# Kernel optimization log

Measured on AMD Instinct MI355X. Metric: run time of the kernel, lower is better.

Reference implementation:

```python
import jax, jax.numpy as jnp
import numpy as np

N, E = 100000, 1600000
IN, HID, NCLS = 128, 128, 64


def setup_inputs() -> dict:
    key = jax.random.key(0)
    ks = jax.random.split(key, 8)
    x = jax.random.normal(ks[0], (N, IN), jnp.float32)
    edge_index = jax.random.randint(ks[1], (2, E), 0, N, dtype=jnp.int32)
    s1 = 1.0 / np.sqrt(IN)
    s2 = 1.0 / np.sqrt(HID)
    return {
        "x": x,
        "edge_index": edge_index,
        "Wl1": jax.random.uniform(ks[2], (IN, HID), jnp.float32, -s1, s1),
        "Wr1": jax.random.uniform(ks[3], (IN, HID), jnp.float32, -s1, s1),
        "b1": jnp.zeros((HID,), jnp.float32),
        "Wl2": jax.random.uniform(ks[4], (HID, NCLS), jnp.float32, -s2, s2),
        "Wr2": jax.random.uniform(ks[5], (HID, NCLS), jnp.float32, -s2, s2),
        "b2": jnp.zeros((NCLS,), jnp.float32),
    }


def _sage_conv(x, src, dst, inv_deg, Wl, Wr, b):
    # mean-aggregate neighbor features at each destination node (PyG SAGEConv)
    agg = jax.ops.segment_sum(x[src], dst, num_segments=N)  # [N, d]
    agg = agg * inv_deg[:, None]
    # out = lin_l(mean_j x_j) + lin_r(x_i); bias lives in lin_l
    return agg @ Wl + x @ Wr + b


def reference(x, edge_index, Wl1, Wr1, b1, Wl2, Wr2, b2):
    src, dst = edge_index[0], edge_index[1]
    deg = jax.ops.segment_sum(jnp.ones((E,), jnp.float32), dst, num_segments=N)
    inv_deg = 1.0 / jnp.maximum(deg, 1.0)
    h = _sage_conv(x, src, dst, inv_deg, Wl1, Wr1, b1)
    h = jax.nn.relu(h)
    # dropout is identity at inference (training=False)
    h = _sage_conv(h, src, dst, inv_deg, Wl2, Wr2, b2)
    return jax.nn.log_softmax(h, axis=1)
```

## Files before the change

kernel.cpp:

```cpp
#include <hip/hip_runtime.h>
#include <hip/hip_bf16.h>


typedef __attribute__((ext_vector_type(8))) short short8;
typedef __attribute__((ext_vector_type(4))) float f32x4;
typedef __attribute__((ext_vector_type(2))) float f32x2;

#define NPB 512
#define BCAP 16384
#define CHUNK 8192

__device__ __forceinline__ ushort f2bf(float f) {
    unsigned u = __float_as_uint(f);
    return (ushort)((u + 0x7fff + ((u >> 16) & 1)) >> 16);
}
__device__ __forceinline__ float bflo(unsigned v) { return __uint_as_float(v << 16); }
__device__ __forceinline__ float bfhi(unsigned v) { return __uint_as_float(v & 0xffff0000u); }
__device__ __forceinline__ unsigned pk4bf(float a, float b) {
    unsigned r;
    asm("v_cvt_pk_bf16_f32 %0, %1, %2" : "=v"(r) : "v"(a), "v"(b));
    return r;
}
__device__ __forceinline__ f32x2 pkadd(f32x2 a, f32x2 b) {
    f32x2 r;
    asm("v_pk_add_f32 %0, %1, %2" : "=v"(r) : "v"(a), "v"(b));
    return r;
}
__device__ __forceinline__ f32x2 shflx2(f32x2 v, int m) {
    f32x2 r; r[0] = __shfl_xor(v[0], m); r[1] = __shfl_xor(v[1], m); return r;
}

__device__ __forceinline__ void wfrag_one(const float* W, ushort* Wf, int i, int COLS) {
    int j = i & 7, m = (i >> 3) & 15, kc = (i >> 7) & 15, ct = i >> 11;
    Wf[i] = f2bf(W[(kc * 8 + j) * COLS + ct * 16 + m]);
}

__global__ void __launch_bounds__(256)
k1_scatter_cvtw(const int* __restrict__ src, const int* __restrict__ dst,
                int* __restrict__ bcount, unsigned* __restrict__ bbuf, int E, int NSC,
                const float* __restrict__ Wl1, const float* __restrict__ Wr1,
                const float* __restrict__ Wl2, const float* __restrict__ Wr2,
                ushort* __restrict__ Wf_l1, ushort* __restrict__ Wf_r1,
                ushort* __restrict__ Wf_l2, ushort* __restrict__ Wf_r2) {
    int tid = threadIdx.x;
    if ((int)blockIdx.x >= NSC) {
        int i = ((int)blockIdx.x - NSC) * 256 + tid;
        if (i < 16384)       wfrag_one(Wl1, Wf_l1, i, 128);
        else if (i < 32768)  wfrag_one(Wr1, Wf_r1, i - 16384, 128);
        else if (i < 40960)  wfrag_one(Wl2, Wf_l2, i - 32768, 64);
        else if (i < 49152)  wfrag_one(Wr2, Wf_r2, i - 40960, 64);
        return;
    }
    __shared__ unsigned entry[CHUNK];
    __shared__ unsigned char ebkt[CHUNK];
    __shared__ int lhist[256], lbase[256], lcur[256];
    lhist[tid] = 0;
    __syncthreads();
    int e0 = blockIdx.x * CHUNK;
    int cnt = min(CHUNK, E - e0);
    int nv = cnt >> 2;
    for (int t = tid; t < nv; t += 256) {
        int4 d4 = ((const int4*)(dst + e0))[t];
        int4 s4 = ((const int4*)(src + e0))[t];
        int i = t * 4;
        int b0 = d4.x >> 9, b1 = d4.y >> 9, b2 = d4.z >> 9, b3 = d4.w >> 9;
        entry[i + 0] = ((unsigned)s4.x << 9) | (unsigned)(d4.x & 511);
        entry[i + 1] = ((unsigned)s4.y << 9) | (unsigned)(d4.y & 511);
        entry[i + 2] = ((unsigned)s4.z << 9) | (unsigned)(d4.z & 511);
        entry[i + 3] = ((unsigned)s4.w << 9) | (unsigned)(d4.w & 511);
        ebkt[i + 0] = (unsigned char)b0; ebkt[i + 1] = (unsigned char)b1;
        ebkt[i + 2] = (unsigned char)b2; ebkt[i + 3] = (unsigned char)b3;
        atomicAdd(&lhist[b0], 1); atomicAdd(&lhist[b1], 1);
        atomicAdd(&lhist[b2], 1); atomicAdd(&lhist[b3], 1);
    }
    for (int i = (nv << 2) + tid; i < cnt; i += 256) {
        int d = dst[e0 + i], s = src[e0 + i];
        int b = d >> 9;
        entry[i] = ((unsigned)s << 9) | (unsigned)(d & 511);
        ebkt[i] = (unsigned char)b;
        atomicAdd(&lhist[b], 1);
    }
    __syncthreads();
    int h = lhist[tid];
    lbase[tid] = (h > 0) ? atomicAdd(&bcount[tid], h) : 0;
    lcur[tid] = 0;
    __syncthreads();
    for (int i = tid; i < cnt; i += 256) {
        int b = ebkt[i];
        int o = atomicAdd(&lcur[b], 1);
        bbuf[(long)b * BCAP + lbase[b] + o] = entry[i];
    }
}

template <int CTOT>
__device__ __forceinline__ void stage_weights(const ushort* __restrict__ Wfl,
                                              const ushort* __restrict__ Wfr,
                                              ushort* dst, int tid) {
    constexpr int HALF = CTOT / 2;
    constexpr int ITERS = (CTOT * 2) / 8192;
#pragma unroll
    for (int r = 0; r < ITERS; ++r) {
        int u = r * 4096 + tid * 8;
        const ushort* s = (u < HALF) ? (Wfl + u) : (Wfr + (u - HALF));
        *(short8*)(dst + u) = *(const short8*)s;
    }
}

template <int COLS, bool F32IN>
__device__ __forceinline__ void proj_tile(int bid, int tid,
                            const void* __restrict__ xin,
                            const ushort* Wl, const ushort* Wr,
                            const float* __restrict__ bias,
                            unsigned char* __restrict__ p8, ushort* __restrict__ q, int N) {
    constexpr int CT = COLS / 16;
    int wave = tid >> 6, lane = tid & 63;
    int quad = lane >> 4, m = lane & 15;
    long row0 = (long)bid * 128 + wave * 16;
    long node = row0 + m;
    long arow = (node < N) ? node : (N - 1);

    f32x4 accp[CT], accq[CT];
#pragma unroll
    for (int ct = 0; ct < CT; ++ct) { accp[ct] = (f32x4)0.0f; accq[ct] = (f32x4)0.0f; }

#pragma unroll
    for (int kk = 0; kk < 128; kk += 32) {
        short8 b;
        if (F32IN) {
            const float* xf = (const float*)xin + arow * 128 + kk + quad * 8;
            float4 f0 = *(const float4*)xf;
            float4 f1 = *(const float4*)(xf + 4);
            union { short8 s; unsigned u[4]; } bu;
            bu.u[0] = pk4bf(f0.x, f0.y);
            bu.u[1] = pk4bf(f0.z, f0.w);
            bu.u[2] = pk4bf(f1.x, f1.y);
            bu.u[3] = pk4bf(f1.z, f1.w);
            b = bu.s;
        } else {
            b = *(const short8*)((const ushort*)xin + arow * 128 + kk + quad * 8);
        }
        int kc = (kk >> 3) + quad;
#pragma unroll
        for (int ct = 0; ct < CT; ++ct) {
            int boff = ((ct * 16 + kc) * 16 + m) * 8;
            short8 al = *(const short8*)(Wl + boff);
            short8 ar = *(const short8*)(Wr + boff);
            accp[ct] = __builtin_amdgcn_mfma_f32_16x16x32_bf16(al, b, accp[ct], 0, 0, 0);
            accq[ct] = __builtin_amdgcn_mfma_f32_16x16x32_bf16(ar, b, accq[ct], 0, 0, 0);
        }
    }

    if (node <= N) {
        unsigned msk = (node == N) ? 0u : ~0u;
#pragma unroll
        for (int ct = 0; ct < CT; ++ct) {
            int c0 = ct * 16 + quad * 4;
            float4 bv = *(const float4*)(bias + c0);
            float q0 = accq[ct][0] + bv.x, q1 = accq[ct][1] + bv.y;
            float q2 = accq[ct][2] + bv.z, q3 = accq[ct][3] + bv.w;
            unsigned w = (unsigned)__builtin_amdgcn_cvt_pk_fp8_f32(accp[ct][0], accp[ct][1], 0, false);
            w = (unsigned)__builtin_amdgcn_cvt_pk_fp8_f32(accp[ct][2], accp[ct][3], (int)w, true);
            *(unsigned*)(p8 + node * COLS + c0) = w & msk;
            uint2 qw; qw.x = pk4bf(q0, q1) & msk; qw.y = pk4bf(q2, q3) & msk;
            *(uint2*)(q + node * COLS + c0) = qw;
        }
    }
}

__global__ void __launch_bounds__(512, 4)
k2_csr_proj1(const unsigned* __restrict__ bbuf, const int* __restrict__ bcount,
             int* __restrict__ rsd,
             float* __restrict__ inv_deg, int* __restrict__ ssrc,
             int NBcsr, int PGRID, int NT, int N,
             const float* __restrict__ x,
             const ushort* __restrict__ Wfl, const ushort* __restrict__ Wfr,
             const float* __restrict__ bias,
             unsigned char* __restrict__ p8, ushort* __restrict__ q) {
    extern __shared__ char smem[];
    int tid = threadIdx.x;
    if ((int)blockIdx.x >= NBcsr) {
        ushort* wsm = (ushort*)smem;
        stage_weights<2 * 128 * 128>(Wfl, Wfr, wsm, tid);
        __syncthreads();
        for (int t = (int)blockIdx.x - NBcsr; t < NT; t += PGRID)
            proj_tile<128, true>(t, tid, x, wsm, wsm + 128 * 128, bias, p8, q, N);
        return;
    }
    int* sdeg = (int*)smem;
    int* lcur = sdeg + NPB;
    int* wsum = lcur + NPB;
    unsigned* ecache = (unsigned*)(wsum + 16);
    const int ECAPV = 3836;
    int b = blockIdx.x;
    int node0 = b * NPB;
    sdeg[tid] = 0;
    __syncthreads();
    int cnt = bcount[b];
    long base = (long)b * BCAP;
    const unsigned* bb = bbuf + base;
    int nv = cnt >> 2;
    int cnv = min(nv, ECAPV);
    for (int t = tid; t < nv; t += 512) {
        uint4 e = ((const uint4*)bb)[t];
        if (t < cnv) ((uint4*)ecache)[t] = e;
        atomicAdd(&sdeg[e.x & 511], 1);
        atomicAdd(&sdeg[e.y & 511], 1);
        atomicAdd(&sdeg[e.z & 511], 1);
        atomicAdd(&sdeg[e.w & 511], 1);
    }
    for (int i = (nv << 2) + tid; i < cnt; i += 512)
        atomicAdd(&sdeg[bb[i] & 511], 1);
    __syncthreads();
    int lane = tid & 63, wv = tid >> 6;
    int c0 = sdeg[tid];
    int dp = (c0 + 15) & ~15;
    int v = dp;
#pragma unroll
    for (int o = 1; o < 64; o <<= 1) {
        int t = __shfl_up(v, o);
        if (lane >= o) v += t;
    }
    if (lane == 63) wsum[wv] = v;
    __syncthreads();
    int add = 0;
    for (int w = 0; w < wv; ++w) add += wsum[w];
    int rs0 = v + add - dp;
    lcur[tid] = rs0;
    if (node0 + tid < N) {
        int2 rv; rv.x = (int)(base + rs0); rv.y = dp;
        *(int2*)(rsd + 2 * (node0 + tid)) = rv;
        inv_deg[node0 + tid] = 1.0f / (float)(c0 > 1 ? c0 : 1);
    }
    __syncthreads();
    for (int t = tid; t < cnv; t += 512) {
        uint4 e = ((const uint4*)ecache)[t];
        int p0 = atomicAdd(&lcur[e.x & 511], 1);
        int p1 = atomicAdd(&lcur[e.y & 511], 1);
        int p2 = atomicAdd(&lcur[e.z & 511], 1);
        int p3 = atomicAdd(&lcur[e.w & 511], 1);
        ssrc[base + p0] = (int)(e.x >> 9);
        ssrc[base + p1] = (int)(e.y >> 9);
        ssrc[base + p2] = (int)(e.z >> 9);
        ssrc[base + p3] = (int)(e.w >> 9);
    }
    for (int t = cnv + tid; t < nv; t += 512) {
        uint4 e = ((const uint4*)bb)[t];
        int p0 = atomicAdd(&lcur[e.x & 511], 1);
        int p1 = atomicAdd(&lcur[e.y & 511], 1);
        int p2 = atomicAdd(&lcur[e.z & 511], 1);
        int p3 = atomicAdd(&lcur[e.w & 511], 1);
        ssrc[base + p0] = (int)(e.x >> 9);
        ssrc[base + p1] = (int)(e.y >> 9);
        ssrc[base + p2] = (int)(e.z >> 9);
        ssrc[base + p3] = (int)(e.w >> 9);
    }
    for (int i = (nv << 2) + tid; i < cnt; i += 512) {
        unsigned w = bb[i];
        int pos = atomicAdd(&lcur[w & 511], 1);
        ssrc[base + pos] = (int)(w >> 9);
    }
    for (int i = c0; i < dp; ++i) ssrc[base + rs0 + i] = N;
    if (tid == 511) {
        int tot = v + add;
        for (int k = 0; k < 16; ++k) ssrc[base + tot + k] = N;
    }
}

__global__ void __launch_bounds__(256)
agg_relu_kernel(const unsigned char* __restrict__ p8,
                const ushort* __restrict__ q,
                const int* __restrict__ ssrc,
                const int* __restrict__ rsd,
                const float* __restrict__ inv_deg,
                ushort* __restrict__ hb, int N) {
    int wave = threadIdx.x >> 6, lane = threadIdx.x & 63;
    int n = blockIdx.x * 4 + wave;
    if (n >= N) return;
    int g = lane >> 4, lm = lane & 15;
    int2 rv = *(const int2*)(rsd + 2 * n);
    int start = rv.x, dp = rv.y;
    float iv = inv_deg[n];
    uint4 qv = make_uint4(0u, 0u, 0u, 0u);
    if (g == 0) qv = *(const uint4*)(q + (long)n * 128 + lm * 8);
    const int* sp = ssrc + start;
    const unsigned char* pb = p8 + lm * 8;
    f32x2 a0 = (f32x2)0.f, a1 = (f32x2)0.f, a2 = (f32x2)0.f, a3 = (f32x2)0.f;
    int4 s = *(const int4*)(sp + 4 * g);
    for (int j = 0; j < dp; j += 16) {
        uint2 v0 = *(const uint2*)(pb + (unsigned)s.x * 128u);
        uint2 v1 = *(const uint2*)(pb + (unsigned)s.y * 128u);
        uint2 v2 = *(const uint2*)(pb + (unsigned)s.z * 128u);
        uint2 v3 = *(const uint2*)(pb + (unsigned)s.w * 128u);
        s = *(const int4*)(sp + j + 16 + 4 * g);
        a0 = pkadd(a0, __builtin_amdgcn_cvt_pk_f32_fp8((int)v0.x, false));
        a1 = pkadd(a1, __builtin_amdgcn_cvt_pk_f32_fp8((int)v0.x, true));
        a2 = pkadd(a2, __builtin_amdgcn_cvt_pk_f32_fp8((int)v0.y, false));
        a3 = pkadd(a3, __builtin_amdgcn_cvt_pk_f32_fp8((int)v0.y, true));
        a0 = pkadd(a0, __builtin_amdgcn_cvt_pk_f32_fp8((int)v1.x, false));
        a1 = pkadd(a1, __builtin_amdgcn_cvt_pk_f32_fp8((int)v1.x, true));
        a2 = pkadd(a2, __builtin_amdgcn_cvt_pk_f32_fp8((int)v1.y, false));
        a3 = pkadd(a3, __builtin_amdgcn_cvt_pk_f32_fp8((int)v1.y, true));
        a0 = pkadd(a0, __builtin_amdgcn_cvt_pk_f32_fp8((int)v2.x, false));
        a1 = pkadd(a1, __builtin_amdgcn_cvt_pk_f32_fp8((int)v2.x, true));
        a2 = pkadd(a2, __builtin_amdgcn_cvt_pk_f32_fp8((int)v2.y, false));
        a3 = pkadd(a3, __builtin_amdgcn_cvt_pk_f32_fp8((int)v2.y, true));
        a0 = pkadd(a0, __builtin_amdgcn_cvt_pk_f32_fp8((int)v3.x, false));
        a1 = pkadd(a1, __builtin_amdgcn_cvt_pk_f32_fp8((int)v3.x, true));
        a2 = pkadd(a2, __builtin_amdgcn_cvt_pk_f32_fp8((int)v3.y, false));
        a3 = pkadd(a3, __builtin_amdgcn_cvt_pk_f32_fp8((int)v3.y, true));
    }
    a0 = pkadd(a0, shflx2(a0, 16)); a1 = pkadd(a1, shflx2(a1, 16));
    a2 = pkadd(a2, shflx2(a2, 16)); a3 = pkadd(a3, shflx2(a3, 16));
    a0 = pkadd(a0, shflx2(a0, 32)); a1 = pkadd(a1, shflx2(a1, 32));
    a2 = pkadd(a2, shflx2(a2, 32)); a3 = pkadd(a3, shflx2(a3, 32));
    if (g == 0) {
        float h0 = fmaxf(a0[0] * iv + bflo(qv.x), 0.f);
        float h1 = fmaxf(a0[1] * iv + bfhi(qv.x), 0.f);
        float h2 = fmaxf(a1[0] * iv + bflo(qv.y), 0.f);
        float h3 = fmaxf(a1[1] * iv + bfhi(qv.y), 0.f);
        float h4 = fmaxf(a2[0] * iv + bflo(qv.z), 0.f);
        float h5 = fmaxf(a2[1] * iv + bfhi(qv.z), 0.f);
        float h6 = fmaxf(a3[0] * iv + bflo(qv.w), 0.f);
        float h7 = fmaxf(a3[1] * iv + bfhi(qv.w), 0.f);
        uint4 hw;
        hw.x = pk4bf(h0, h1); hw.y = pk4bf(h2, h3);
        hw.z = pk4bf(h4, h5); hw.w = pk4bf(h6, h7);
        *(uint4*)(hb + (long)n * 128 + lm * 8) = hw;
    }
}

__global__ void __launch_bounds__(512, 4)
proj2_kernel(const ushort* __restrict__ hb,
             const ushort* __restrict__ Wfl, const ushort* __restrict__ Wfr,
             const float* __restrict__ bias,
             unsigned char* __restrict__ u8, ushort* __restrict__ v, int N) {
    __shared__ ushort wsm[2 * 64 * 128];
    stage_weights<2 * 64 * 128>(Wfl, Wfr, wsm, (int)threadIdx.x);
    __syncthreads();
    proj_tile<64, false>((int)blockIdx.x, (int)threadIdx.x, hb, wsm, wsm + 64 * 128,
                         bias, u8, v, N);
}

__global__ void __launch_bounds__(256)
agg_lsm_kernel(const unsigned char* __restrict__ u8,
               const ushort* __restrict__ v,
               const int* __restrict__ ssrc,
               const int* __restrict__ rsd,
               const float* __restrict__ inv_deg,
               float* __restrict__ out, int N) {
    int wave = threadIdx.x >> 6, lane = threadIdx.x & 63;
    int n = blockIdx.x * 4 + wave;
    if (n >= N) return;
    int g = lane >> 4, lm = lane & 15;
    int2 rv = *(const int2*)(rsd + 2 * n);
    int start = rv.x, dp = rv.y;
    float iv = inv_deg[n];
    uint2 vv2 = *(const uint2*)(v + (long)n * 64 + lm * 4);
    const int* sp = ssrc + start;
    const unsigned char* ub = u8 + lm * 4;
    f32x2 a0 = (f32x2)0.f, a1 = (f32x2)0.f;
    int4 s = *(const int4*)(sp + 4 * g);
    for (int j = 0; j < dp; j += 16) {
        unsigned v0 = *(const unsigned*)(ub + (unsigned)s.x * 64u);
        unsigned v1 = *(const unsigned*)(ub + (unsigned)s.y * 64u);
        unsigned v2 = *(const unsigned*)(ub + (unsigned)s.z * 64u);
        unsigned v3 = *(const unsigned*)(ub + (unsigned)s.w * 64u);
        s = *(const int4*)(sp + j + 16 + 4 * g);
        a0 = pkadd(a0, __builtin_amdgcn_cvt_pk_f32_fp8((int)v0, false));
        a1 = pkadd(a1, __builtin_amdgcn_cvt_pk_f32_fp8((int)v0, true));
        a0 = pkadd(a0, __builtin_amdgcn_cvt_pk_f32_fp8((int)v1, false));
        a1 = pkadd(a1, __builtin_amdgcn_cvt_pk_f32_fp8((int)v1, true));
        a0 = pkadd(a0, __builtin_amdgcn_cvt_pk_f32_fp8((int)v2, false));
        a1 = pkadd(a1, __builtin_amdgcn_cvt_pk_f32_fp8((int)v2, true));
        a0 = pkadd(a0, __builtin_amdgcn_cvt_pk_f32_fp8((int)v3, false));
        a1 = pkadd(a1, __builtin_amdgcn_cvt_pk_f32_fp8((int)v3, true));
    }
    a0 = pkadd(a0, shflx2(a0, 16)); a1 = pkadd(a1, shflx2(a1, 16));
    a0 = pkadd(a0, shflx2(a0, 32)); a1 = pkadd(a1, shflx2(a1, 32));

    float z0 = a0[0] * iv + bflo(vv2.x), z1 = a0[1] * iv + bfhi(vv2.x);
    float z2 = a1[0] * iv + bflo(vv2.y), z3 = a1[1] * iv + bfhi(vv2.y);
    float mx = fmaxf(fmaxf(z0, z1), fmaxf(z2, z3));
#pragma unroll
    for (int o = 8; o > 0; o >>= 1) mx = fmaxf(mx, __shfl_xor(mx, o));
    float e = (__expf(z0 - mx) + __expf(z1 - mx)) + (__expf(z2 - mx) + __expf(z3 - mx));
#pragma unroll
    for (int o = 8; o > 0; o >>= 1) e += __shfl_xor(e, o);
    float ls = mx + __logf(e);
    if (g == 0) {
        float4 o0;
        o0.x = z0 - ls; o0.y = z1 - ls; o0.z = z2 - ls; o0.w = z3 - ls;
        *(float4*)(out + (long)n * 64 + lm * 4) = o0;
    }
}

extern "C" void kernel_launch(void* const* d_in, const int* in_sizes, int n_in,
                              void* d_out, int out_size, void* d_ws, size_t ws_size,
                              hipStream_t stream) {
    const float* x   = (const float*)d_in[0];
    const int*   ei  = (const int*)d_in[1];
    const float* Wl1 = (const float*)d_in[2];
    const float* Wr1 = (const float*)d_in[3];
    const float* b1  = (const float*)d_in[4];
    const float* Wl2 = (const float*)d_in[5];
    const float* Wr2 = (const float*)d_in[6];
    const float* b2  = (const float*)d_in[7];

    const int N = in_sizes[0] / 128;
    const int E = in_sizes[1] / 2;
    const int* src = ei;
    const int* dst = ei + E;
    const int NB = (N + NPB - 1) / NPB;
    const int NSC = (E + CHUNK - 1) / CHUNK;

    size_t off = 0;
    auto take = [&](size_t nbytes) -> void* {
        void* ptr = (void*)((char*)d_ws + off);
        off += (nbytes + 255) & ~(size_t)255;
        return ptr;
    };
    int*      bcount    = (int*)take((size_t)NB * 4);
    unsigned* bbuf      = (unsigned*)take((size_t)NB * BCAP * 4);
    int*      rsd       = (int*)take((size_t)N * 8);
    float*    inv_deg   = (float*)take((size_t)N * 4);
    int*      ssrc      = (int*)take((size_t)NB * BCAP * 4);
    unsigned char* p8   = (unsigned char*)take((size_t)(N + 1) * 128);
    ushort*   q         = (ushort*)take((size_t)(N + 1) * 128 * 2);
    ushort*   hb        = (ushort*)take((size_t)N * 128 * 2);
    ushort*   Wf_l1     = (ushort*)take(128 * 128 * 2);
    ushort*   Wf_r1     = (ushort*)take(128 * 128 * 2);
    ushort*   Wf_l2     = (ushort*)take(64 * 128 * 2);
    ushort*   Wf_r2     = (ushort*)take(64 * 128 * 2);
    unsigned char* u8 = p8;
    ushort*        v  = q;
    (void)ws_size; (void)n_in; (void)out_size;

    static bool attr_set = false;
    if (!attr_set) {
        hipFuncSetAttribute((const void*)k2_csr_proj1,
                            hipFuncAttributeMaxDynamicSharedMemorySize, 65536);
        attr_set = true;
    }

    hipMemsetAsync(bcount, 0, (size_t)NB * 4, stream);

    k1_scatter_cvtw<<<NSC + 192, 256, 0, stream>>>(src, dst, bcount, bbuf, E, NSC,
                                                   Wl1, Wr1, Wl2, Wr2,
                                                   Wf_l1, Wf_r1, Wf_l2, Wf_r2);

    const int PGRID = 316;
    const int NT = (N + 127) / 128;
    k2_csr_proj1<<<NB + PGRID, 512, 65536, stream>>>(bbuf, bcount, rsd, inv_deg, ssrc,
                                                     NB, PGRID, NT, N, x,
                                                     Wf_l1, Wf_r1, b1, p8, q);

    agg_relu_kernel<<<(N + 3) / 4, 256, 0, stream>>>(p8, q, ssrc, rsd, inv_deg, hb, N);

    proj2_kernel<<<(N + 127) / 128, 512, 0, stream>>>(hb, Wf_l2, Wf_r2, b2, u8, v, N);
    agg_lsm_kernel<<<(N + 3) / 4, 256, 0, stream>>>(u8, v, ssrc, rsd, inv_deg,
                                                    (float*)d_out, N);
}
```

Baseline: 246.9 us.

## Pre-convert x to bf16 in scatter kernel and use one projection tile per block

The fp32-to-bf16 conversion of x moves out of the layer-1 projection and into extra blocks of the first scatter kernel, which write a bf16 copy of x. The projection blocks in the CSR kernel then read bf16 directly, and the persistent grid of 316 blocks looping over tiles becomes one block per 128-row tile. This shortens the projection tiles that overlap with CSR construction. In exchange, 256 blocks must stream the full 51 MB x tensor and write a 25 MB bf16 copy inside the scatter kernel, which adds total traffic and workspace.

Result: no change. 247.1 us (+0.1%).

```diff
diff --git a/kernel.cpp b/kernel.cpp
--- a/kernel.cpp
+++ b/kernel.cpp
@@ -41,7 +41,8 @@
                 const float* __restrict__ Wl1, const float* __restrict__ Wr1,
                 const float* __restrict__ Wl2, const float* __restrict__ Wr2,
                 ushort* __restrict__ Wf_l1, ushort* __restrict__ Wf_r1,
-                ushort* __restrict__ Wf_l2, ushort* __restrict__ Wf_r2) {
+                ushort* __restrict__ Wf_l2, ushort* __restrict__ Wf_r2,
+                const float* __restrict__ x, ushort* __restrict__ xb, int N) {
     int tid = threadIdx.x;
     if ((int)blockIdx.x >= NSC) {
         int i = ((int)blockIdx.x - NSC) * 256 + tid;
@@ -49,6 +50,15 @@
         else if (i < 32768)  wfrag_one(Wr1, Wf_r1, i - 16384, 128);
         else if (i < 40960)  wfrag_one(Wl2, Wf_l2, i - 32768, 64);
         else if (i < 49152)  wfrag_one(Wr2, Wf_r2, i - 40960, 64);
+        const long TOT = (long)N * 128;
+        for (long e = (long)i * 8; e < TOT; e += (long)256 * 256 * 8) {
+            float4 f0 = *(const float4*)(x + e);
+            float4 f1 = *(const float4*)(x + e + 4);
+            union { short8 s; unsigned u[4]; } bu;
+            bu.u[0] = pk4bf(f0.x, f0.y); bu.u[1] = pk4bf(f0.z, f0.w);
+            bu.u[2] = pk4bf(f1.x, f1.y); bu.u[3] = pk4bf(f1.z, f1.w);
+            *(short8*)(xb + e) = bu.s;
+        }
         return;
     }
     __shared__ unsigned entry[CHUNK];
@@ -106,9 +116,9 @@
     }
 }
 
-template <int COLS, bool F32IN>
+template <int COLS>
 __device__ __forceinline__ void proj_tile(int bid, int tid,
-                            const void* __restrict__ xin,
+                            const ushort* __restrict__ xin,
                             const ushort* Wl, const ushort* Wr,
                             const float* __restrict__ bias,
                             unsigned char* __restrict__ p8, ushort* __restrict__ q, int N) {
@@ -125,20 +135,7 @@
 
 #pragma unroll
     for (int kk = 0; kk < 128; kk += 32) {
-        short8 b;
-        if (F32IN) {
-            const float* xf = (const float*)xin + arow * 128 + kk + quad * 8;
-            float4 f0 = *(const float4*)xf;
-            float4 f1 = *(const float4*)(xf + 4);
-            union { short8 s; unsigned u[4]; } bu;
-            bu.u[0] = pk4bf(f0.x, f0.y);
-            bu.u[1] = pk4bf(f0.z, f0.w);
-            bu.u[2] = pk4bf(f1.x, f1.y);
-            bu.u[3] = pk4bf(f1.z, f1.w);
-            b = bu.s;
-        } else {
-            b = *(const short8*)((const ushort*)xin + arow * 128 + kk + quad * 8);
-        }
+        short8 b = *(const short8*)(xin + arow * 128 + kk + quad * 8);
         int kc = (kk >> 3) + quad;
 #pragma unroll
         for (int ct = 0; ct < CT; ++ct) {
@@ -171,8 +168,8 @@
 k2_csr_proj1(const unsigned* __restrict__ bbuf, const int* __restrict__ bcount,
              int* __restrict__ rsd,
              float* __restrict__ inv_deg, int* __restrict__ ssrc,
-             int NBcsr, int PGRID, int NT, int N,
-             const float* __restrict__ x,
+             int NBcsr, int N,
+             const ushort* __restrict__ xb,
              const ushort* __restrict__ Wfl, const ushort* __restrict__ Wfr,
              const float* __restrict__ bias,
              unsigned char* __restrict__ p8, ushort* __restrict__ q) {
@@ -182,8 +179,8 @@
         ushort* wsm = (ushort*)smem;
         stage_weights<2 * 128 * 128>(Wfl, Wfr, wsm, tid);
         __syncthreads();
-        for (int t = (int)blockIdx.x - NBcsr; t < NT; t += PGRID)
-            proj_tile<128, true>(t, tid, x, wsm, wsm + 128 * 128, bias, p8, q, N);
+        proj_tile<128>((int)blockIdx.x - NBcsr, tid, xb, wsm, wsm + 128 * 128,
+                       bias, p8, q, N);
         return;
     }
     int* sdeg = (int*)smem;
@@ -337,8 +334,8 @@
     __shared__ ushort wsm[2 * 64 * 128];
     stage_weights<2 * 64 * 128>(Wfl, Wfr, wsm, (int)threadIdx.x);
     __syncthreads();
-    proj_tile<64, false>((int)blockIdx.x, (int)threadIdx.x, hb, wsm, wsm + 64 * 128,
-                         bias, u8, v, N);
+    proj_tile<64>((int)blockIdx.x, (int)threadIdx.x, hb, wsm, wsm + 64 * 128,
+                  bias, u8, v, N);
 }
 
 __global__ void __launch_bounds__(256)
@@ -424,6 +421,7 @@
     int*      rsd       = (int*)take((size_t)N * 8);
     float*    inv_deg   = (float*)take((size_t)N * 4);
     int*      ssrc      = (int*)take((size_t)NB * BCAP * 4);
+    ushort*   xb        = (ushort*)take((size_t)N * 128 * 2);
     unsigned char* p8   = (unsigned char*)take((size_t)(N + 1) * 128);
     ushort*   q         = (ushort*)take((size_t)(N + 1) * 128 * 2);
     ushort*   hb        = (ushort*)take((size_t)N * 128 * 2);
@@ -444,15 +442,14 @@
 
     hipMemsetAsync(bcount, 0, (size_t)NB * 4, stream);
 
-    k1_scatter_cvtw<<<NSC + 192, 256, 0, stream>>>(src, dst, bcount, bbuf, E, NSC,
+    k1_scatter_cvtw<<<NSC + 256, 256, 0, stream>>>(src, dst, bcount, bbuf, E, NSC,
                                                    Wl1, Wr1, Wl2, Wr2,
-                                                   Wf_l1, Wf_r1, Wf_l2, Wf_r2);
-
-    const int PGRID = 316;
-    const int NT = (N + 127) / 128;
-    k2_csr_proj1<<<NB + PGRID, 512, 65536, stream>>>(bbuf, bcount, rsd, inv_deg, ssrc,
-                                                     NB, PGRID, NT, N, x,
-                                                     Wf_l1, Wf_r1, b1, p8, q);
+                                                   Wf_l1, Wf_r1, Wf_l2, Wf_r2,
+                                                   x, xb, N);
+
+    int P1 = (N + 127) / 128;
+    k2_csr_proj1<<<NB + P1, 512, 65536, stream>>>(bbuf, bcount, rsd, inv_deg, ssrc,
+                                                  NB, N, xb, Wf_l1, Wf_r1, b1, p8, q);
 
     agg_relu_kernel<<<(N + 3) / 4, 256, 0, stream>>>(p8, q, ssrc, rsd, inv_deg, hb, N);
 
```

## Overlap layer-1 projection with edge scatter instead of CSR build

Applied to the files above, without the earlier changes.

Moves weight conversion into its own small kernel. The layer-1 projection blocks are co-scheduled with the edge bucket-scatter kernel instead of the CSR-building kernel, using one projection tile per block instead of a persistent grid. The scatter kernel moves to 512 threads and dynamic shared memory so both roles share one launch. The aim is to rebalance which stages overlap, at the cost of an extra launch and a different occupancy mix.

Result: no change. 246.9 us (-0.0%).

```diff
diff --git a/kernel.cpp b/kernel.cpp
--- a/kernel.cpp
+++ b/kernel.cpp
@@ -35,31 +35,120 @@
     Wf[i] = f2bf(W[(kc * 8 + j) * COLS + ct * 16 + m]);
 }
 
-__global__ void __launch_bounds__(256)
-k1_scatter_cvtw(const int* __restrict__ src, const int* __restrict__ dst,
-                int* __restrict__ bcount, unsigned* __restrict__ bbuf, int E, int NSC,
-                const float* __restrict__ Wl1, const float* __restrict__ Wr1,
-                const float* __restrict__ Wl2, const float* __restrict__ Wr2,
-                ushort* __restrict__ Wf_l1, ushort* __restrict__ Wf_r1,
-                ushort* __restrict__ Wf_l2, ushort* __restrict__ Wf_r2) {
+__global__ void __launch_bounds__(512)
+k0_cvtw(const float* __restrict__ Wl1, const float* __restrict__ Wr1,
+        const float* __restrict__ Wl2, const float* __restrict__ Wr2,
+        ushort* __restrict__ Wf_l1, ushort* __restrict__ Wf_r1,
+        ushort* __restrict__ Wf_l2, ushort* __restrict__ Wf_r2) {
+    int i = (int)blockIdx.x * 512 + (int)threadIdx.x;
+    if (i < 16384)       wfrag_one(Wl1, Wf_l1, i, 128);
+    else if (i < 32768)  wfrag_one(Wr1, Wf_r1, i - 16384, 128);
+    else if (i < 40960)  wfrag_one(Wl2, Wf_l2, i - 32768, 64);
+    else if (i < 49152)  wfrag_one(Wr2, Wf_r2, i - 40960, 64);
+}
+
+template <int CTOT>
+__device__ __forceinline__ void stage_weights(const ushort* __restrict__ Wfl,
+                                              const ushort* __restrict__ Wfr,
+                                              ushort* dst, int tid) {
+    constexpr int HALF = CTOT / 2;
+    constexpr int ITERS = (CTOT * 2) / 8192;
+#pragma unroll
+    for (int r = 0; r < ITERS; ++r) {
+        int u = r * 4096 + tid * 8;
+        const ushort* s = (u < HALF) ? (Wfl + u) : (Wfr + (u - HALF));
+        *(short8*)(dst + u) = *(const short8*)s;
+    }
+}
+
+template <int COLS, bool F32IN>
+__device__ __forceinline__ void proj_tile(int bid, int tid,
+                            const void* __restrict__ xin,
+                            const ushort* Wl, const ushort* Wr,
+                            const float* __restrict__ bias,
+                            unsigned char* __restrict__ p8, ushort* __restrict__ q, int N) {
+    constexpr int CT = COLS / 16;
+    int wave = tid >> 6, lane = tid & 63;
+    int quad = lane >> 4, m = lane & 15;
+    long row0 = (long)bid * 128 + wave * 16;
+    long node = row0 + m;
+    long arow = (node < N) ? node : (N - 1);
+
+    f32x4 accp[CT], accq[CT];
+#pragma unroll
+    for (int ct = 0; ct < CT; ++ct) { accp[ct] = (f32x4)0.0f; accq[ct] = (f32x4)0.0f; }
+
+#pragma unroll
+    for (int kk = 0; kk < 128; kk += 32) {
+        short8 b;
+        if (F32IN) {
+            const float* xf = (const float*)xin + arow * 128 + kk + quad * 8;
+            float4 f0 = *(const float4*)xf;
+            float4 f1 = *(const float4*)(xf + 4);
+            union { short8 s; unsigned u[4]; } bu;
+            bu.u[0] = pk4bf(f0.x, f0.y); bu.u[1] = pk4bf(f0.z, f0.w);
+            bu.u[2] = pk4bf(f1.x, f1.y); bu.u[3] = pk4bf(f1.z, f1.w);
+            b = bu.s;
+        } else {
+            b = *(const short8*)((const ushort*)xin + arow * 128 + kk + quad * 8);
+        }
+        int kc = (kk >> 3) + quad;
+#pragma unroll
+        for (int ct = 0; ct < CT; ++ct) {
+            int boff = ((ct * 16 + kc) * 16 + m) * 8;
+            short8 al = *(const short8*)(Wl + boff);
+            short8 ar = *(const short8*)(Wr + boff);
+            accp[ct] = __builtin_amdgcn_mfma_f32_16x16x32_bf16(al, b, accp[ct], 0, 0, 0);
+            accq[ct] = __builtin_amdgcn_mfma_f32_16x16x32_bf16(ar, b, accq[ct], 0, 0, 0);
+        }
+    }
+
+    if (node <= N) {
+        unsigned msk = (node == N) ? 0u : ~0u;
+#pragma unroll
+        for (int ct = 0; ct < CT; ++ct) {
+            int c0 = ct * 16 + quad * 4;
+            float4 bv = *(const float4*)(bias + c0);
+            float q0 = accq[ct][0] + bv.x, q1 = accq[ct][1] + bv.y;
+            float q2 = accq[ct][2] + bv.z, q3 = accq[ct][3] + bv.w;
+            unsigned w = (unsigned)__builtin_amdgcn_cvt_pk_fp8_f32(accp[ct][0], accp[ct][1], 0, false);
+            w = (unsigned)__builtin_amdgcn_cvt_pk_fp8_f32(accp[ct][2], accp[ct][3], (int)w, true);
+            *(unsigned*)(p8 + node * COLS + c0) = w & msk;
+            uint2 qw; qw.x = pk4bf(q0, q1) & msk; qw.y = pk4bf(q2, q3) & msk;
+            *(uint2*)(q + node * COLS + c0) = qw;
+        }
+    }
+}
+
+__global__ void __launch_bounds__(512, 4)
+k1_scatter_proj1(const int* __restrict__ src, const int* __restrict__ dst,
+                 int* __restrict__ bcount, unsigned* __restrict__ bbuf,
+                 int E, int NSC, int N,
+                 const float* __restrict__ x,
+                 const ushort* __restrict__ Wfl, const ushort* __restrict__ Wfr,
+                 const float* __restrict__ bias,
+                 unsigned char* __restrict__ p8, ushort* __restrict__ q) {
+    extern __shared__ char smem[];
     int tid = threadIdx.x;
     if ((int)blockIdx.x >= NSC) {
-        int i = ((int)blockIdx.x - NSC) * 256 + tid;
-        if (i < 16384)       wfrag_one(Wl1, Wf_l1, i, 128);
-        else if (i < 32768)  wfrag_one(Wr1, Wf_r1, i - 16384, 128);
-        else if (i < 40960)  wfrag_one(Wl2, Wf_l2, i - 32768, 64);
-        else if (i < 49152)  wfrag_one(Wr2, Wf_r2, i - 40960, 64);
+        ushort* wsm = (ushort*)smem;
+        stage_weights<2 * 128 * 128>(Wfl, Wfr, wsm, tid);
+        __syncthreads();
+        proj_tile<128, true>((int)blockIdx.x - NSC, tid, x, wsm, wsm + 128 * 128,
+                             bias, p8, q, N);
         return;
     }
-    __shared__ unsigned entry[CHUNK];
-    __shared__ unsigned char ebkt[CHUNK];
-    __shared__ int lhist[256], lbase[256], lcur[256];
-    lhist[tid] = 0;
+    unsigned* entry = (unsigned*)smem;
+    unsigned char* ebkt = (unsigned char*)(entry + CHUNK);
+    int* lhist = (int*)(ebkt + CHUNK);
+    int* lbase = lhist + 256;
+    int* lcur  = lbase + 256;
+    if (tid < 256) lhist[tid] = 0;
     __syncthreads();
     int e0 = blockIdx.x * CHUNK;
     int cnt = min(CHUNK, E - e0);
     int nv = cnt >> 2;
-    for (int t = tid; t < nv; t += 256) {
+    for (int t = tid; t < nv; t += 512) {
         int4 d4 = ((const int4*)(dst + e0))[t];
         int4 s4 = ((const int4*)(src + e0))[t];
         int i = t * 4;
@@ -73,7 +162,7 @@
         atomicAdd(&lhist[b0], 1); atomicAdd(&lhist[b1], 1);
         atomicAdd(&lhist[b2], 1); atomicAdd(&lhist[b3], 1);
     }
-    for (int i = (nv << 2) + tid; i < cnt; i += 256) {
+    for (int i = (nv << 2) + tid; i < cnt; i += 512) {
         int d = dst[e0 + i], s = src[e0 + i];
         int b = d >> 9;
         entry[i] = ((unsigned)s << 9) | (unsigned)(d & 511);
@@ -81,111 +170,25 @@
         atomicAdd(&lhist[b], 1);
     }
     __syncthreads();
-    int h = lhist[tid];
-    lbase[tid] = (h > 0) ? atomicAdd(&bcount[tid], h) : 0;
-    lcur[tid] = 0;
-    __syncthreads();
-    for (int i = tid; i < cnt; i += 256) {
+    if (tid < 256) {
+        int h = lhist[tid];
+        lbase[tid] = (h > 0) ? atomicAdd(&bcount[tid], h) : 0;
+        lcur[tid] = 0;
+    }
+    __syncthreads();
+    for (int i = tid; i < cnt; i += 512) {
         int b = ebkt[i];
         int o = atomicAdd(&lcur[b], 1);
         bbuf[(long)b * BCAP + lbase[b] + o] = entry[i];
     }
 }
 
-template <int CTOT>
-__device__ __forceinline__ void stage_weights(const ushort* __restrict__ Wfl,
-                                              const ushort* __restrict__ Wfr,
-                                              ushort* dst, int tid) {
-    constexpr int HALF = CTOT / 2;
-    constexpr int ITERS = (CTOT * 2) / 8192;
-#pragma unroll
-    for (int r = 0; r < ITERS; ++r) {
-        int u = r * 4096 + tid * 8;
-        const ushort* s = (u < HALF) ? (Wfl + u) : (Wfr + (u - HALF));
-        *(short8*)(dst + u) = *(const short8*)s;
-    }
-}
-
-template <int COLS, bool F32IN>
-__device__ __forceinline__ void proj_tile(int bid, int tid,
-                            const void* __restrict__ xin,
-                            const ushort* Wl, const ushort* Wr,
-                            const float* __restrict__ bias,
-                            unsigned char* __restrict__ p8, ushort* __restrict__ q, int N) {
-    constexpr int CT = COLS / 16;
-    int wave = tid >> 6, lane = tid & 63;
-    int quad = lane >> 4, m = lane & 15;
-    long row0 = (long)bid * 128 + wave * 16;
-    long node = row0 + m;
-    long arow = (node < N) ? node : (N - 1);
-
-    f32x4 accp[CT], accq[CT];
-#pragma unroll
-    for (int ct = 0; ct < CT; ++ct) { accp[ct] = (f32x4)0.0f; accq[ct] = (f32x4)0.0f; }
-
-#pragma unroll
-    for (int kk = 0; kk < 128; kk += 32) {
-        short8 b;
-        if (F32IN) {
-            const float* xf = (const float*)xin + arow * 128 + kk + quad * 8;
-            float4 f0 = *(const float4*)xf;
-            float4 f1 = *(const float4*)(xf + 4);
-            union { short8 s; unsigned u[4]; } bu;
-            bu.u[0] = pk4bf(f0.x, f0.y);
-            bu.u[1] = pk4bf(f0.z, f0.w);
-            bu.u[2] = pk4bf(f1.x, f1.y);
-            bu.u[3] = pk4bf(f1.z, f1.w);
-            b = bu.s;
-        } else {
-            b = *(const short8*)((const ushort*)xin + arow * 128 + kk + quad * 8);
-        }
-        int kc = (kk >> 3) + quad;
-#pragma unroll
-        for (int ct = 0; ct < CT; ++ct) {
-            int boff = ((ct * 16 + kc) * 16 + m) * 8;
-            short8 al = *(const short8*)(Wl + boff);
-            short8 ar = *(const short8*)(Wr + boff);
-            accp[ct] = __builtin_amdgcn_mfma_f32_16x16x32_bf16(al, b, accp[ct], 0, 0, 0);
-            accq[ct] = __builtin_amdgcn_mfma_f32_16x16x32_bf16(ar, b, accq[ct], 0, 0, 0);
-        }
-    }
-
-    if (node <= N) {
-        unsigned msk = (node == N) ? 0u : ~0u;
-#pragma unroll
-        for (int ct = 0; ct < CT; ++ct) {
-            int c0 = ct * 16 + quad * 4;
-            float4 bv = *(const float4*)(bias + c0);
-            float q0 = accq[ct][0] + bv.x, q1 = accq[ct][1] + bv.y;
-            float q2 = accq[ct][2] + bv.z, q3 = accq[ct][3] + bv.w;
-            unsigned w = (unsigned)__builtin_amdgcn_cvt_pk_fp8_f32(accp[ct][0], accp[ct][1], 0, false);
-            w = (unsigned)__builtin_amdgcn_cvt_pk_fp8_f32(accp[ct][2], accp[ct][3], (int)w, true);
-            *(unsigned*)(p8 + node * COLS + c0) = w & msk;
-            uint2 qw; qw.x = pk4bf(q0, q1) & msk; qw.y = pk4bf(q2, q3) & msk;
-            *(uint2*)(q + node * COLS + c0) = qw;
-        }
-    }
-}
-
 __global__ void __launch_bounds__(512, 4)
-k2_csr_proj1(const unsigned* __restrict__ bbuf, const int* __restrict__ bcount,
-             int* __restrict__ rsd,
-             float* __restrict__ inv_deg, int* __restrict__ ssrc,
-             int NBcsr, int PGRID, int NT, int N,
-             const float* __restrict__ x,
-             const ushort* __restrict__ Wfl, const ushort* __restrict__ Wfr,
-             const float* __restrict__ bias,
-             unsigned char* __restrict__ p8, ushort* __restrict__ q) {
+k2_csr(const unsigned* __restrict__ bbuf, const int* __restrict__ bcount,
+       int* __restrict__ rsd,
+       float* __restrict__ inv_deg, int* __restrict__ ssrc, int N) {
     extern __shared__ char smem[];
     int tid = threadIdx.x;
-    if ((int)blockIdx.x >= NBcsr) {
-        ushort* wsm = (ushort*)smem;
-        stage_weights<2 * 128 * 128>(Wfl, Wfr, wsm, tid);
-        __syncthreads();
-        for (int t = (int)blockIdx.x - NBcsr; t < NT; t += PGRID)
-            proj_tile<128, true>(t, tid, x, wsm, wsm + 128 * 128, bias, p8, q, N);
-        return;
-    }
     int* sdeg = (int*)smem;
     int* lcur = sdeg + NPB;
     int* wsum = lcur + NPB;
@@ -437,22 +440,23 @@
 
     static bool attr_set = false;
     if (!attr_set) {
-        hipFuncSetAttribute((const void*)k2_csr_proj1,
+        hipFuncSetAttribute((const void*)k1_scatter_proj1,
+                            hipFuncAttributeMaxDynamicSharedMemorySize, 65536);
+        hipFuncSetAttribute((const void*)k2_csr,
                             hipFuncAttributeMaxDynamicSharedMemorySize, 65536);
         attr_set = true;
     }
 
     hipMemsetAsync(bcount, 0, (size_t)NB * 4, stream);
 
-    k1_scatter_cvtw<<<NSC + 192, 256, 0, stream>>>(src, dst, bcount, bbuf, E, NSC,
-                                                   Wl1, Wr1, Wl2, Wr2,
-                                                   Wf_l1, Wf_r1, Wf_l2, Wf_r2);
-
-    const int PGRID = 316;
-    const int NT = (N + 127) / 128;
-    k2_csr_proj1<<<NB + PGRID, 512, 65536, stream>>>(bbuf, bcount, rsd, inv_deg, ssrc,
-                                                     NB, PGRID, NT, N, x,
-                                                     Wf_l1, Wf_r1, b1, p8, q);
+    k0_cvtw<<<96, 512, 0, stream>>>(Wl1, Wr1, Wl2, Wr2, Wf_l1, Wf_r1, Wf_l2, Wf_r2);
+
+    int P1 = (N + 127) / 128;
+    k1_scatter_proj1<<<NSC + P1, 512, 65536, stream>>>(src, dst, bcount, bbuf,
+                                                       E, NSC, N, x,
+                                                       Wf_l1, Wf_r1, b1, p8, q);
+
+    k2_csr<<<NB, 512, 65536, stream>>>(bbuf, bcount, rsd, inv_deg, ssrc, N);
 
     agg_relu_kernel<<<(N + 3) / 4, 256, 0, stream>>>(p8, q, ssrc, rsd, inv_deg, hb, N);
 
```
